# Optimization experiments

Measured on AMD Instinct MI355X. Metric: run time of the kernel, lower is better.

## Reference

```python
import jax, jax.numpy as jnp
import numpy as np

# dims: batch, seq_len(N)=hidden(H) (required: layer>0 feeds H back into Linears sized N),
# features C, AATE dim A, layers L, decoder widths
B, N, C, A, H, L, FC, FFC = 256, 512, 64, 64, 512, 3, 256, 32


def setup_inputs() -> dict:
    key = jax.random.key(0)
    ks = jax.random.split(key, 24)
    def p(k, shape):
        return jax.random.normal(k, shape, jnp.float32) * 0.02
    return dict(
        x=jax.random.normal(ks[0], (B, N, C), jnp.float32),
        occ=jax.random.normal(ks[1], (B, N, 1), jnp.float32),
        proj_w=p(ks[2], (A, N)), proj_b=p(ks[3], (A,)),
        ll1_w=p(ks[4], (L, A, N)), ll1_b=p(ks[5], (L, A)),
        ll2_w=p(ks[6], (L, A, N)), ll2_b=p(ks[7], (L, A)),
        g1_w=p(ks[8], (L, 1, N + A)), g1_b=p(ks[9], (L, 1)),
        g2_w=p(ks[10], (L, 1, N + A)), g2_b=p(ks[11], (L, 1)),
        gc_w=p(ks[12], (L, H, 3 * N)), gc_b=p(ks[13], (L, H)),
        ta_w=p(ks[14], (H, H)), ta_b=p(ks[15], (H,)),
        d1_w=p(ks[16], (FC, H)), d1_b=p(ks[17], (FC,)),
        d2_w=p(ks[18], (1, FC)), d2_b=p(ks[19], (1,)),
        c1_w=p(ks[20], (FFC, C)), c1_b=p(ks[21], (FFC,)),
        c2_w=p(ks[22], (1, FFC)), c2_b=p(ks[23], (1,)),
    )


def _nconv(x, a):
    # x: [B,F,n,m], a: [B,m,n,v] -> [B,F,v,m]   (torch.einsum('bfnm,bmnv->bfvm'))
    return jnp.einsum('bfnm,bmnv->bfvm', x, a)


def reference(x, occ, proj_w, proj_b, ll1_w, ll1_b, ll2_w, ll2_b,
              g1_w, g1_b, g2_w, g2_b, gc_w, gc_b, ta_w, ta_b,
              d1_w, d1_b, d2_w, d2_b, c1_w, c1_b, c2_w, c2_b):
    Bn, Nn, Cn = x.shape
    An = proj_w.shape[0]
    xm = jnp.transpose(x, (0, 2, 1))[:, :, None, :]               # [B,C,1,N]  (M=1)
    proj = jnp.transpose(occ, (0, 2, 1)) @ proj_w.T + proj_b      # [B,1,A]
    # torch: repeat(M,1,C,1).view(B,M,C,A) -> tile along C; view(B,M,A,C) reinterleaves
    AATE = jnp.tile(proj[:, :, None, :], (1, 1, Cn, 1))           # [B,1,C,A]
    AATE_T = AATE.reshape(Bn, 1, An, Cn)                          # [B,1,A,C] (raw reshape, as in torch .view)
    for l in range(L):
        a_pc = jnp.transpose(AATE, (0, 2, 1, 3))                  # [B,C,1,A]
        at_pc = jnp.transpose(AATE_T, (0, 3, 1, 2))               # [B,C,1,A]
        m1 = jax.nn.relu(jnp.tanh(jnp.concatenate([xm, a_pc], -1) @ g1_w[l].T + g1_b[l]))   # [B,C,1,1]
        m2 = jax.nn.relu(jnp.tanh(jnp.concatenate([xm, at_pc], -1) @ g2_w[l].T + g2_b[l]))  # [B,C,1,1]
        e1 = jax.nn.softmax(jax.nn.relu(m1 * (xm @ ll1_w[l].T + ll1_b[l])), axis=-1)        # [B,C,1,A]
        e2 = jax.nn.softmax(jax.nn.relu(m2 * (xm @ ll2_w[l].T + ll2_b[l])), axis=-1)        # [B,C,1,A]
        e1 = AATE + jnp.transpose(e1, (0, 2, 1, 3))               # [B,1,C,A]
        e2 = AATE_T + jnp.transpose(e2, (0, 2, 3, 1))             # [B,1,A,C]
        adp = jax.nn.softmax(jax.nn.relu(e1 @ e2), axis=-1)       # [B,1,C,C] adaptive adjacency
        xg = jnp.transpose(xm, (0, 3, 1, 2))                      # [B,N,C,1]
        x1 = _nconv(xg, adp)
        x2 = _nconv(x1, adp)
        h = jnp.concatenate([xg, x1, x2], axis=1)                 # [B,3N,C,1]
        hh = jnp.einsum('bfcm,of->bocm', h, gc_w[l]) + gc_b[l][None, :, None, None]  # [B,H,C,1]
        xnew = jnp.transpose(jax.nn.relu(hh), (0, 2, 3, 1))       # [B,C,1,H]
        xm = (xm + xnew) if l > 0 else xnew                       # residual for layer>0
    z = xm.mean(axis=2)                                           # [B,C,H]  (mean over M=1)
    z = z @ ta_w.T + ta_b                                         # temporal_agg (Linear)
    d = jax.nn.relu(z @ d1_w.T + d1_b) @ d2_w.T + d2_b            # decoder -> [B,C,1]
    dp = jnp.transpose(d, (0, 2, 1))                              # [B,1,C]
    cd = jax.nn.relu(dp @ c1_w.T + c1_b) @ c2_w.T + c2_b          # channel_decoder -> [B,1,1]
    return jnp.abs(jnp.transpose(cd, (0, 2, 1)).squeeze(-1))      # [B,1] rul_prediction
```

## Files before the change

kernel.cpp:

```cpp
#include <hip/hip_runtime.h>

typedef unsigned short u16;
typedef __attribute__((ext_vector_type(8))) short short8;
typedef __attribute__((ext_vector_type(4))) float f32x4;


__device__ __forceinline__ u16 f2b(float f) {
    union { float f; unsigned int i; } v; v.f = f;
    unsigned int x = v.i;
    x += 0x7fffu + ((x >> 16) & 1u);
    return (u16)(x >> 16);
}
__device__ __forceinline__ float b2f(u16 u) {
    union { unsigned int i; float f; } v;
    v.i = ((unsigned int)u) << 16;
    return v.f;
}
__device__ __forceinline__ void gl_lds16(const u16* g, u16* l) {
    __builtin_amdgcn_global_load_lds((__attribute__((address_space(1))) void*)(u16*)g,
                                     (__attribute__((address_space(3))) void*)l, 16, 0, 0);
}

__global__ __launch_bounds__(256) void k_cvt(const float* __restrict__ src, u16* __restrict__ dst, int n4) {
    int i = blockIdx.x * 256 + threadIdx.x;
    if (i < n4) {
        float4 v = ((const float4*)src)[i];
        ushort4 o; o.x = f2b(v.x); o.y = f2b(v.y); o.z = f2b(v.z); o.w = f2b(v.w);
        ((ushort4*)dst)[i] = o;
    }
}

__global__ __launch_bounds__(256) void k_transpose(const float* __restrict__ x, float* __restrict__ xm,
                                                   u16* __restrict__ xmb) {
    __shared__ float tile[64][65];
    const int b  = blockIdx.y;
    const int n0 = blockIdx.x * 64;
    const int t  = threadIdx.x;
    const int c  = t & 63;
    const int dn = t >> 6;
#pragma unroll
    for (int i = 0; i < 16; ++i) {
        int nl = dn + i * 4;
        tile[c][nl] = x[((size_t)b * 512 + n0 + nl) * 64 + c];
    }
    __syncthreads();
    const int nl = t & 63;
    const int cb = (t >> 6) * 16;
#pragma unroll
    for (int i = 0; i < 16; ++i) {
        int c2 = cb + i;
        float v = tile[c2][nl];
        size_t idx = ((size_t)b * 64 + c2) * 512 + n0 + nl;
        xm[idx] = v;
        xmb[idx] = f2b(v);
    }
}

__global__ __launch_bounds__(64) void k_proj(const float* __restrict__ occ, const float* __restrict__ pw,
                                             const float* __restrict__ pb, float* __restrict__ proj) {
    const int b = blockIdx.x;
    const int a = threadIdx.x;
    const float* ob = occ + (size_t)b * 512;
    const float* wr = pw + (size_t)a * 512;
    float acc = 0.f;
    for (int n = 0; n < 512; ++n) acc += ob[n] * wr[n];
    proj[b * 64 + a] = acc + pb[a];
}

__global__ __launch_bounds__(64) void k_pm(const u16* __restrict__ xmb,
                                           const float* __restrict__ g1w, const float* __restrict__ g1b,
                                           const float* __restrict__ g2w, const float* __restrict__ g2b,
                                           const float* __restrict__ proj, float* __restrict__ vb) {
    const int r = blockIdx.x;
    const int b = r >> 6, c = r & 63;
    const int lane = threadIdx.x;
    const u16* row = xmb + (size_t)r * 512 + lane * 8;
    uint4 xv = *(const uint4*)row;
    const u16* xp = (const u16*)&xv;
    float4 w1a = *(const float4*)(g1w + lane * 8);
    float4 w1b = *(const float4*)(g1w + lane * 8 + 4);
    float4 w2a = *(const float4*)(g2w + lane * 8);
    float4 w2b = *(const float4*)(g2w + lane * 8 + 4);
    float g1v[8] = {w1a.x, w1a.y, w1a.z, w1a.w, w1b.x, w1b.y, w1b.z, w1b.w};
    float g2v[8] = {w2a.x, w2a.y, w2a.z, w2a.w, w2b.x, w2b.y, w2b.z, w2b.w};
    float a1 = 0.f, a2 = 0.f;
#pragma unroll
    for (int e = 0; e < 8; ++e) {
        float xvf = b2f(xp[e]);
        a1 += xvf * g1v[e];
        a2 += xvf * g2v[e];
    }
    a1 += proj[b * 64 + lane] * g1w[512 + lane];
    a2 += proj[b * 64 + c]    * g2w[512 + lane];
    for (int off = 32; off; off >>= 1) { a1 += __shfl_xor(a1, off); a2 += __shfl_xor(a2, off); }
    float m1 = tanhf(a1 + g1b[0]); m1 = m1 > 0.f ? m1 : 0.f;
    float m2 = tanhf(a2 + g2b[0]); m2 = m2 > 0.f ? m2 : 0.f;
    const int a = lane;
    float s1 = m1 * vb[(size_t)r * 128 + a];       s1 = s1 > 0.f ? s1 : 0.f;
    float s2 = m2 * vb[(size_t)r * 128 + 64 + a];  s2 = s2 > 0.f ? s2 : 0.f;
    float mx1 = s1, mx2 = s2;
    for (int off = 32; off; off >>= 1) { mx1 = fmaxf(mx1, __shfl_xor(mx1, off)); mx2 = fmaxf(mx2, __shfl_xor(mx2, off)); }
    float e1 = expf(s1 - mx1), e2 = expf(s2 - mx2);
    float su1 = e1, su2 = e2;
    for (int off = 32; off; off >>= 1) { su1 += __shfl_xor(su1, off); su2 += __shfl_xor(su2, off); }
    vb[(size_t)r * 128 + a]      = proj[b * 64 + a] + e1 / su1;
    vb[(size_t)r * 128 + 64 + a] = proj[b * 64 + c] + e2 / su2;
}

__global__ __launch_bounds__(256) void k_adp(const float* __restrict__ vb, u16* __restrict__ adpT) {
    __shared__ float P1s[64][64];
    __shared__ float P2s[64][65];
    __shared__ __align__(16) u16 Tl[64 * 72];
    const int b = blockIdx.x;
    const int t = threadIdx.x;
#pragma unroll
    for (int i = 0; i < 16; ++i) {
        int idx = t + 256 * i;
        int c = idx >> 6, a = idx & 63;
        P1s[c][a] = vb[((size_t)b * 64 + c) * 128 + a];
        P2s[c][a] = vb[((size_t)b * 64 + c) * 128 + 64 + a];
    }
    __syncthreads();
    const int lane = t & 63;
    const int w = t >> 6;
    for (int ci = 0; ci < 16; ++ci) {
        int c = w + ci * 4;
        float s = 0.f;
        for (int a = 0; a < 64; ++a) s += P1s[c][a] * P2s[lane][a];
        s = fmaxf(s, 0.f);
        float mx = s;
        for (int off = 32; off; off >>= 1) mx = fmaxf(mx, __shfl_xor(mx, off));
        float e = expf(s - mx);
        float su = e;
        for (int off = 32; off; off >>= 1) su += __shfl_xor(su, off);
        Tl[lane * 72 + c] = f2b(e / su);
    }
    __syncthreads();
    const int v = t >> 2, ck = (t & 3) * 16;
    u16* dst = adpT + ((size_t)b * 64 + v) * 64 + ck;
    *(uint4*)dst       = *(const uint4*)&Tl[v * 72 + ck];
    *(uint4*)(dst + 8) = *(const uint4*)&Tl[v * 72 + ck + 8];
}

__global__ __launch_bounds__(256) void k_nconv2(const u16* __restrict__ Xbf, const u16* __restrict__ adpT,
                                                u16* __restrict__ x1bf, u16* __restrict__ x2bf) {
    __shared__ __align__(16) u16 Ts[64 * 72];
    __shared__ __align__(16) u16 Xs[128 * 72];
    const int b  = blockIdx.y;
    const int n0 = blockIdx.x * 128;
    const int t  = threadIdx.x;
    const int lane = t & 63, w = t >> 6;
    const int lrow = lane & 15, q = lane >> 4;
    const int wn = w * 32;

    {
        int v = t >> 2, ck = (t & 3) * 8;
        const u16* src = adpT + ((size_t)b * 64 + v) * 64;
        *(uint4*)&Ts[v * 72 + ck]      = *(const uint4*)(src + ck);
        *(uint4*)&Ts[v * 72 + ck + 32] = *(const uint4*)(src + ck + 32);
    }
    {
        int c = t >> 2;
        const u16* xr = Xbf + ((size_t)b * 64 + c) * 512 + n0;
#pragma unroll
        for (int j = 0; j < 4; ++j) {
            int nn = j * 32 + (t & 3) * 8;
            uint4 vv = *(const uint4*)(xr + nn);
            const u16* pv = (const u16*)&vv;
#pragma unroll
            for (int e = 0; e < 8; ++e) Xs[(nn + e) * 72 + c] = pv[e];
        }
    }
    __syncthreads();

    const f32x4 zero = {0.f, 0.f, 0.f, 0.f};
    f32x4 acc[4][2];
#pragma unroll
    for (int mt = 0; mt < 4; ++mt)
#pragma unroll
        for (int nt = 0; nt < 2; ++nt) acc[mt][nt] = zero;

#pragma unroll
    for (int ks = 0; ks < 2; ++ks) {
        short8 af[4], bfr[2];
#pragma unroll
        for (int mt = 0; mt < 4; ++mt) af[mt]  = *(const short8*)&Ts[(mt * 16 + lrow) * 72 + ks * 32 + q * 8];
#pragma unroll
        for (int nt = 0; nt < 2; ++nt) bfr[nt] = *(const short8*)&Xs[(wn + nt * 16 + lrow) * 72 + ks * 32 + q * 8];
#pragma unroll
        for (int mt = 0; mt < 4; ++mt)
#pragma unroll
            for (int nt = 0; nt < 2; ++nt)
                acc[mt][nt] = __builtin_amdgcn_mfma_f32_16x16x32_bf16(af[mt], bfr[nt], acc[mt][nt], 0, 0, 0);
    }
    __syncthreads();

#pragma unroll
    for (int mt = 0; mt < 4; ++mt)
#pragma unroll
        for (int nt = 0; nt < 2; ++nt) {
            int nl = wn + nt * 16 + lrow;
            ushort4 u;
            u.x = f2b(acc[mt][nt][0]); u.y = f2b(acc[mt][nt][1]);
            u.z = f2b(acc[mt][nt][2]); u.w = f2b(acc[mt][nt][3]);
            *(ushort4*)&Xs[nl * 72 + mt * 16 + q * 4] = u;
#pragma unroll
            for (int i = 0; i < 4; ++i)
                x1bf[((size_t)(b * 64 + mt * 16 + q * 4 + i)) * 512 + n0 + nl] = ((const u16*)&u)[i];
        }
    __syncthreads();

    f32x4 acc2[4][2];
#pragma unroll
    for (int mt = 0; mt < 4; ++mt)
#pragma unroll
        for (int nt = 0; nt < 2; ++nt) acc2[mt][nt] = zero;
#pragma unroll
    for (int ks = 0; ks < 2; ++ks) {
        short8 af[4], bfr[2];
#pragma unroll
        for (int mt = 0; mt < 4; ++mt) af[mt]  = *(const short8*)&Ts[(mt * 16 + lrow) * 72 + ks * 32 + q * 8];
#pragma unroll
        for (int nt = 0; nt < 2; ++nt) bfr[nt] = *(const short8*)&Xs[(wn + nt * 16 + lrow) * 72 + ks * 32 + q * 8];
#pragma unroll
        for (int mt = 0; mt < 4; ++mt)
#pragma unroll
            for (int nt = 0; nt < 2; ++nt)
                acc2[mt][nt] = __builtin_amdgcn_mfma_f32_16x16x32_bf16(af[mt], bfr[nt], acc2[mt][nt], 0, 0, 0);
    }
#pragma unroll
    for (int mt = 0; mt < 4; ++mt)
#pragma unroll
        for (int nt = 0; nt < 2; ++nt) {
            int nl = wn + nt * 16 + lrow;
#pragma unroll
            for (int i = 0; i < 4; ++i)
                x2bf[((size_t)(b * 64 + mt * 16 + q * 4 + i)) * 512 + n0 + nl] = f2b(acc2[mt][nt][i]);
        }
}

template<int BM, int BN>
__global__ __launch_bounds__(256) void mfma_gemm(
    const u16* __restrict__ A0, const u16* __restrict__ A1, const u16* __restrict__ A2,
    const u16* __restrict__ W0, const u16* __restrict__ W1, int nsplit,
    const float* __restrict__ bias0, const float* __restrict__ bias1,
    const float* __restrict__ res, float* __restrict__ out, u16* __restrict__ outbf,
    int N, int K, int relu)
{
    constexpr int MT = BM / 32;
    constexpr int NT = BN / 32;
    constexpr int AI = BM / 16;
    constexpr int BI = BN / 16;
    constexpr int TILE = (BM + BN) * 32;
    __shared__ __align__(16) u16 SM[2 * TILE];
    const int t    = threadIdx.x;
    const int m0   = blockIdx.x * BM;
    const int n0   = blockIdx.y * BN;
    const int lane = t & 63;
    const int w    = t >> 6;
    const int wm   = (w >> 1) * (BM / 2);
    const int wn   = (w & 1) * (BN / 2);
    const int lrow = lane & 15;
    const int q    = lane >> 4;
    const int sr16 = lane >> 2;
    const int sp   = lane & 3;

    auto stage = [&](int k0, int buf) {
        u16* As = SM + buf * TILE;
        u16* Bs = As + BM * 32;
        const u16* Abase = A0;
        int kloc = k0;
        if (K > 512) {
            int seg = k0 >> 9;
            Abase = (seg == 0) ? A0 : ((seg == 1) ? A1 : A2);
            kloc = k0 & 511;
        }
#pragma unroll
        for (int jj = 0; jj < AI / 4; ++jj) {
            int j = jj * 4 + w;
            int row = j * 16 + sr16;
            int c = (sp - (row >> 1)) & 3;
            gl_lds16(Abase + (size_t)(m0 + row) * 512 + kloc + c * 8, As + j * 512);
        }
#pragma unroll
        for (int jj = 0; jj < BI / 4; ++jj) {
            int j = jj * 4 + w;
            int row = j * 16 + sr16;
            int n = n0 + row;
            const u16* wr = (n < nsplit) ? (W0 + (size_t)n * K) : (W1 + (size_t)(n - nsplit) * K);
            int c = (sp - (row >> 1)) & 3;
            gl_lds16(wr + k0 + c * 8, Bs + j * 512);
        }
    };

    const f32x4 zero = {0.f, 0.f, 0.f, 0.f};
    f32x4 acc[MT][NT];
#pragma unroll
    for (int i = 0; i < MT; ++i)
#pragma unroll
        for (int j = 0; j < NT; ++j) acc[i][j] = zero;

    stage(0, 0);
    const int iters = K >> 5;
    int buf = 0;
    for (int it = 0; it < iters; ++it) {
        __syncthreads();
        if (it + 1 < iters) stage((it + 1) * 32, buf ^ 1);
        const u16* As = SM + buf * TILE;
        const u16* Bs = As + BM * 32;
        short8 af[MT], bfr[NT];
#pragma unroll
        for (int mt = 0; mt < MT; ++mt) {
            int row = wm + mt * 16 + lrow;
            int p = (q + (row >> 1)) & 3;
            af[mt] = *(const short8*)&As[row * 32 + p * 8];
        }
#pragma unroll
        for (int nt = 0; nt < NT; ++nt) {
            int row = wn + nt * 16 + lrow;
            int p = (q + (row >> 1)) & 3;
            bfr[nt] = *(const short8*)&Bs[row * 32 + p * 8];
        }
#pragma unroll
        for (int mt = 0; mt < MT; ++mt)
#pragma unroll
            for (int nt = 0; nt < NT; ++nt)
                acc[mt][nt] = __builtin_amdgcn_mfma_f32_16x16x32_bf16(af[mt], bfr[nt], acc[mt][nt], 0, 0, 0);
        buf ^= 1;
    }

#pragma unroll
    for (int mt = 0; mt < MT; ++mt) {
        int mb = m0 + wm + mt * 16 + q * 4;
#pragma unroll
        for (int nt = 0; nt < NT; ++nt) {
            int n = n0 + wn + nt * 16 + lrow;
            float bvv = (n < nsplit) ? bias0[n] : bias1[n - nsplit];
#pragma unroll
            for (int i = 0; i < 4; ++i) {
                float v = acc[mt][nt][i] + bvv;
                if (relu) v = fmaxf(v, 0.f);
                if (res) v += res[(size_t)(mb + i) * N + n];
                if (out) out[(size_t)(mb + i) * N + n] = v;
                if (outbf) outbf[(size_t)(mb + i) * N + n] = f2b(v);
            }
        }
    }
}

__global__ __launch_bounds__(256) void k_dvec(const float* __restrict__ tmat, const float* __restrict__ d2w,
                                              const float* __restrict__ d2b, float* __restrict__ dvec) {
    const int r = blockIdx.x * 4 + (threadIdx.x >> 6);
    const int lane = threadIdx.x & 63;
    const float* row = tmat + (size_t)r * 256;
    float acc = 0.f;
    for (int f = lane; f < 256; f += 64) acc += row[f] * d2w[f];
    for (int off = 32; off; off >>= 1) acc += __shfl_xor(acc, off);
    if (lane == 0) dvec[r] = acc + d2b[0];
}

__global__ __launch_bounds__(64) void k_final(const float* __restrict__ dvec, const float* __restrict__ c1w,
                                              const float* __restrict__ c1b, const float* __restrict__ c2w,
                                              const float* __restrict__ c2b, float* __restrict__ out) {
    const int b = blockIdx.x;
    const int f = threadIdx.x;
    float part = 0.f;
    if (f < 32) {
        float acc = c1b[f];
        const float* dr = dvec + b * 64;
        for (int c = 0; c < 64; ++c) acc += dr[c] * c1w[f * 64 + c];
        acc = acc > 0.f ? acc : 0.f;
        part = acc * c2w[f];
    }
    for (int off = 32; off; off >>= 1) part += __shfl_xor(part, off);
    if (f == 0) out[b] = fabsf(part + c2b[0]);
}

extern "C" void kernel_launch(void* const* d_in, const int* in_sizes, int n_in,
                              void* d_out, int out_size, void* d_ws, size_t ws_size,
                              hipStream_t stream) {
    const float* x     = (const float*)d_in[0];
    const float* occ   = (const float*)d_in[1];
    const float* projw = (const float*)d_in[2];
    const float* projb = (const float*)d_in[3];
    const float* ll1w  = (const float*)d_in[4];
    const float* ll1b  = (const float*)d_in[5];
    const float* ll2w  = (const float*)d_in[6];
    const float* ll2b  = (const float*)d_in[7];
    const float* g1w   = (const float*)d_in[8];
    const float* g1b   = (const float*)d_in[9];
    const float* g2w   = (const float*)d_in[10];
    const float* g2b   = (const float*)d_in[11];
    const float* gcw   = (const float*)d_in[12];
    const float* gcb   = (const float*)d_in[13];
    const float* taw   = (const float*)d_in[14];
    const float* tab   = (const float*)d_in[15];
    const float* d1w   = (const float*)d_in[16];
    const float* d1b   = (const float*)d_in[17];
    const float* d2w   = (const float*)d_in[18];
    const float* d2b   = (const float*)d_in[19];
    const float* c1w   = (const float*)d_in[20];
    const float* c1b   = (const float*)d_in[21];
    const float* c2w   = (const float*)d_in[22];
    const float* c2b   = (const float*)d_in[23];

    const size_t MR = (size_t)16384 * 512;
    float* ws   = (float*)d_ws;
    float* xmA  = ws;
    float* xmB  = xmA + MR;
    float* x2T  = xmB + MR;
    float* vbuf = x2T + MR;
    float* proj = vbuf + (size_t)16384 * 128;
    float* m1m2 = proj + 16384;
    float* dvec = m1m2 + 32768;
    u16* bfb     = (u16*)(dvec + 16384);
    u16* xmA_bf  = bfb;
    u16* xmB_bf  = xmA_bf + MR;
    u16* x1_bf   = xmB_bf + MR;
    u16* x2_bf   = x1_bf + MR;
    u16* x1T_bf  = x2_bf + MR;
    u16* adpT_bf = x1T_bf + MR;
    u16* ll1w_bf = adpT_bf + (size_t)16384 * 64;
    u16* ll2w_bf = ll1w_bf + 98304;
    u16* gcw_bf  = ll2w_bf + 98304;
    u16* taw_bf  = gcw_bf + 2359296;
    u16* d1w_bf  = taw_bf + 262144;

    k_cvt<<<96,   256, 0, stream>>>(ll1w, ll1w_bf, 98304 / 4);
    k_cvt<<<96,   256, 0, stream>>>(ll2w, ll2w_bf, 98304 / 4);
    k_cvt<<<2304, 256, 0, stream>>>(gcw,  gcw_bf,  2359296 / 4);
    k_cvt<<<256,  256, 0, stream>>>(taw,  taw_bf,  262144 / 4);
    k_cvt<<<128,  256, 0, stream>>>(d1w,  d1w_bf,  131072 / 4);

    k_transpose<<<dim3(8, 256), 256, 0, stream>>>(x, xmA, xmA_bf);
    k_proj<<<256, 64, 0, stream>>>(occ, projw, projb, proj);

    float* cur = xmA;  u16* cur_bf = xmA_bf;
    float* nxt = xmB;  u16* nxt_bf = xmB_bf;
    for (int l = 0; l < 3; ++l) {
        mfma_gemm<64, 64><<<dim3(256, 2), 256, 0, stream>>>(
            cur_bf, nullptr, nullptr,
            ll1w_bf + (size_t)l * 32768, ll2w_bf + (size_t)l * 32768, 64,
            ll1b + l * 64, ll2b + l * 64, nullptr, vbuf, nullptr, 128, 512, 0);
        k_pm<<<16384, 64, 0, stream>>>(cur_bf, g1w + l * 576, g1b + l, g2w + l * 576, g2b + l, proj, vbuf);
        k_adp<<<256, 256, 0, stream>>>(vbuf, adpT_bf);
        k_nconv2<<<dim3(4, 256), 256, 0, stream>>>(cur_bf, adpT_bf, x1_bf, x2_bf);
        mfma_gemm<128, 64><<<dim3(128, 8), 256, 0, stream>>>(
            cur_bf, x1_bf, x2_bf,
            gcw_bf + (size_t)l * 786432, gcw_bf + (size_t)l * 786432, 512,
            gcb + l * 512, gcb + l * 512, (l > 0 ? cur : nullptr), nxt, nxt_bf, 512, 1536, 1);
        { float* tf = cur; cur = nxt; nxt = tf; }
        { u16* tb = cur_bf; cur_bf = nxt_bf; nxt_bf = tb; }
    }
    mfma_gemm<128, 64><<<dim3(128, 8), 256, 0, stream>>>(
        cur_bf, nullptr, nullptr, taw_bf, taw_bf, 512, tab, tab, nullptr, nullptr, x1T_bf, 512, 512, 0);
    mfma_gemm<64, 64><<<dim3(256, 4), 256, 0, stream>>>(
        x1T_bf, nullptr, nullptr, d1w_bf, d1w_bf, 256, d1b, d1b, nullptr, x2T, nullptr, 256, 512, 1);
    k_dvec<<<4096, 256, 0, stream>>>(x2T, d2w, d2b, dvec);
    k_final<<<256, 64, 0, stream>>>(dvec, c1w, c1b, c2w, c2b, (float*)d_out);
}
```

Before: 477.1 us.

## Drop fp32 activation copies, use bf16 residual, and deepen GEMM K-step to 64

The transpose and the GCN GEMM no longer write fp32 copies of the activations. The residual is now read from the bf16 activation buffer, which removes a large fp32 write and read stream in each layer. The GEMM main loop also stages two 32-wide K chunks per barrier, halving the number of synchronisations at the cost of doubled shared memory. Accumulating the residual from bf16 adds rounding error to the residual path.

```diff
diff --git a/kernel.cpp b/kernel.cpp
--- a/kernel.cpp
+++ b/kernel.cpp
@@ -30,8 +30,7 @@
     }
 }
 
-__global__ __launch_bounds__(256) void k_transpose(const float* __restrict__ x, float* __restrict__ xm,
-                                                   u16* __restrict__ xmb) {
+__global__ __launch_bounds__(256) void k_transpose(const float* __restrict__ x, u16* __restrict__ xmb) {
     __shared__ float tile[64][65];
     const int b  = blockIdx.y;
     const int n0 = blockIdx.x * 64;
@@ -49,10 +48,7 @@
 #pragma unroll
     for (int i = 0; i < 16; ++i) {
         int c2 = cb + i;
-        float v = tile[c2][nl];
-        size_t idx = ((size_t)b * 64 + c2) * 512 + n0 + nl;
-        xm[idx] = v;
-        xmb[idx] = f2b(v);
+        xmb[((size_t)b * 64 + c2) * 512 + n0 + nl] = f2b(tile[c2][nl]);
     }
 }
 
@@ -244,15 +240,15 @@
     const u16* __restrict__ A0, const u16* __restrict__ A1, const u16* __restrict__ A2,
     const u16* __restrict__ W0, const u16* __restrict__ W1, int nsplit,
     const float* __restrict__ bias0, const float* __restrict__ bias1,
-    const float* __restrict__ res, float* __restrict__ out, u16* __restrict__ outbf,
+    const u16* __restrict__ resbf, float* __restrict__ out, u16* __restrict__ outbf,
     int N, int K, int relu)
 {
     constexpr int MT = BM / 32;
     constexpr int NT = BN / 32;
     constexpr int AI = BM / 16;
     constexpr int BI = BN / 16;
-    constexpr int TILE = (BM + BN) * 32;
-    __shared__ __align__(16) u16 SM[2 * TILE];
+    constexpr int CH = (BM + BN) * 32;
+    __shared__ __align__(16) u16 SM[4 * CH];
     const int t    = threadIdx.x;
     const int m0   = blockIdx.x * BM;
     const int n0   = blockIdx.y * BN;
@@ -265,8 +261,8 @@
     const int sr16 = lane >> 2;
     const int sp   = lane & 3;
 
-    auto stage = [&](int k0, int buf) {
-        u16* As = SM + buf * TILE;
+    auto stage32 = [&](int k0, int buf, int ch) {
+        u16* As = SM + (buf * 2 + ch) * CH;
         u16* Bs = As + BM * 32;
         const u16* Abase = A0;
         int kloc = k0;
@@ -300,32 +296,39 @@
 #pragma unroll
         for (int j = 0; j < NT; ++j) acc[i][j] = zero;
 
-    stage(0, 0);
-    const int iters = K >> 5;
+    stage32(0, 0, 0);
+    stage32(32, 0, 1);
+    const int iters = K >> 6;
     int buf = 0;
     for (int it = 0; it < iters; ++it) {
         __syncthreads();
-        if (it + 1 < iters) stage((it + 1) * 32, buf ^ 1);
-        const u16* As = SM + buf * TILE;
-        const u16* Bs = As + BM * 32;
-        short8 af[MT], bfr[NT];
-#pragma unroll
-        for (int mt = 0; mt < MT; ++mt) {
-            int row = wm + mt * 16 + lrow;
-            int p = (q + (row >> 1)) & 3;
-            af[mt] = *(const short8*)&As[row * 32 + p * 8];
-        }
-#pragma unroll
-        for (int nt = 0; nt < NT; ++nt) {
-            int row = wn + nt * 16 + lrow;
-            int p = (q + (row >> 1)) & 3;
-            bfr[nt] = *(const short8*)&Bs[row * 32 + p * 8];
-        }
-#pragma unroll
-        for (int mt = 0; mt < MT; ++mt)
-#pragma unroll
-            for (int nt = 0; nt < NT; ++nt)
-                acc[mt][nt] = __builtin_amdgcn_mfma_f32_16x16x32_bf16(af[mt], bfr[nt], acc[mt][nt], 0, 0, 0);
+        if (it + 1 < iters) {
+            stage32((it + 1) * 64, buf ^ 1, 0);
+            stage32((it + 1) * 64 + 32, buf ^ 1, 1);
+        }
+#pragma unroll
+        for (int ch = 0; ch < 2; ++ch) {
+            const u16* As = SM + (buf * 2 + ch) * CH;
+            const u16* Bs = As + BM * 32;
+            short8 af[MT], bfr[NT];
+#pragma unroll
+            for (int mt = 0; mt < MT; ++mt) {
+                int row = wm + mt * 16 + lrow;
+                int p = (q + (row >> 1)) & 3;
+                af[mt] = *(const short8*)&As[row * 32 + p * 8];
+            }
+#pragma unroll
+            for (int nt = 0; nt < NT; ++nt) {
+                int row = wn + nt * 16 + lrow;
+                int p = (q + (row >> 1)) & 3;
+                bfr[nt] = *(const short8*)&Bs[row * 32 + p * 8];
+            }
+#pragma unroll
+            for (int mt = 0; mt < MT; ++mt)
+#pragma unroll
+                for (int nt = 0; nt < NT; ++nt)
+                    acc[mt][nt] = __builtin_amdgcn_mfma_f32_16x16x32_bf16(af[mt], bfr[nt], acc[mt][nt], 0, 0, 0);
+        }
         buf ^= 1;
     }
 
@@ -340,7 +343,7 @@
             for (int i = 0; i < 4; ++i) {
                 float v = acc[mt][nt][i] + bvv;
                 if (relu) v = fmaxf(v, 0.f);
-                if (res) v += res[(size_t)(mb + i) * N + n];
+                if (resbf) v += b2f(resbf[(size_t)(mb + i) * N + n]);
                 if (out) out[(size_t)(mb + i) * N + n] = v;
                 if (outbf) outbf[(size_t)(mb + i) * N + n] = f2b(v);
             }
@@ -406,13 +409,10 @@
 
     const size_t MR = (size_t)16384 * 512;
     float* ws   = (float*)d_ws;
-    float* xmA  = ws;
-    float* xmB  = xmA + MR;
-    float* x2T  = xmB + MR;
-    float* vbuf = x2T + MR;
+    float* x2T  = ws;
+    float* vbuf = x2T + (size_t)16384 * 256;
     float* proj = vbuf + (size_t)16384 * 128;
-    float* m1m2 = proj + 16384;
-    float* dvec = m1m2 + 32768;
+    float* dvec = proj + 16384;
     u16* bfb     = (u16*)(dvec + 16384);
     u16* xmA_bf  = bfb;
     u16* xmB_bf  = xmA_bf + MR;
@@ -432,11 +432,11 @@
     k_cvt<<<256,  256, 0, stream>>>(taw,  taw_bf,  262144 / 4);
     k_cvt<<<128,  256, 0, stream>>>(d1w,  d1w_bf,  131072 / 4);
 
-    k_transpose<<<dim3(8, 256), 256, 0, stream>>>(x, xmA, xmA_bf);
+    k_transpose<<<dim3(8, 256), 256, 0, stream>>>(x, xmA_bf);
     k_proj<<<256, 64, 0, stream>>>(occ, projw, projb, proj);
 
-    float* cur = xmA;  u16* cur_bf = xmA_bf;
-    float* nxt = xmB;  u16* nxt_bf = xmB_bf;
+    u16* cur_bf = xmA_bf;
+    u16* nxt_bf = xmB_bf;
     for (int l = 0; l < 3; ++l) {
         mfma_gemm<64, 64><<<dim3(256, 2), 256, 0, stream>>>(
             cur_bf, nullptr, nullptr,
@@ -448,8 +448,7 @@
         mfma_gemm<128, 64><<<dim3(128, 8), 256, 0, stream>>>(
             cur_bf, x1_bf, x2_bf,
             gcw_bf + (size_t)l * 786432, gcw_bf + (size_t)l * 786432, 512,
-            gcb + l * 512, gcb + l * 512, (l > 0 ? cur : nullptr), nxt, nxt_bf, 512, 1536, 1);
-        { float* tf = cur; cur = nxt; nxt = tf; }
+            gcb + l * 512, gcb + l * 512, (l > 0 ? cur_bf : nullptr), nullptr, nxt_bf, 512, 1536, 1);
         { u16* tb = cur_bf; cur_bf = nxt_bf; nxt_bf = tb; }
     }
     mfma_gemm<128, 64><<<dim3(128, 8), 256, 0, stream>>>(
```

After: 488.3 us. 2.3% more time.
